# Performance work log

Measured on AMD Instinct MI355X. Metric: run time of the kernel, lower is better.

## Reference

```python
import jax, jax.numpy as jnp
import numpy as np

ND, ED, HD, L, K = 128, 64, 256, 4, 24   # node_dim, edge_dim(num_rbf), hidden_dim, num_layers, max_neighbors
CUTOFF = 8.0
N = 2048  # n_atoms


def _silu(x):
    return x * jax.nn.sigmoid(x)


def _lattice(lengths, angles):
    a, b, c = lengths[0], lengths[1], lengths[2]
    deg = jnp.asarray(np.pi / 180.0, lengths.dtype)
    al, be, ga = angles[0] * deg, angles[1] * deg, angles[2] * deg
    lx = a
    xy = b * jnp.cos(ga)
    xz = c * jnp.cos(be)
    ly = b * jnp.sin(ga)
    yz = (b * c * jnp.cos(al) - xy * xz) / ly
    lz = jnp.sqrt(c ** 2 - xz ** 2 - yz ** 2)
    z = jnp.zeros((), lengths.dtype)
    return jnp.stack([jnp.stack([lx, z, z]), jnp.stack([xy, ly, z]), jnp.stack([xz, yz, lz])])


def _rbf(d):
    centers = jnp.linspace(0.0, CUTOFF, ED)
    widths = jnp.full((ED,), CUTOFF / ED)
    d = d[..., None]
    g = jnp.exp(-(d - centers) ** 2 / (2.0 * widths ** 2))
    cv = 0.5 * (jnp.cos(d * jnp.pi / CUTOFF) + 1.0) * (d < CUTOFF).astype(d.dtype)
    return g * cv


def _forward(atom_types, frac_coords, lengths, angles, timesteps, emb, tW, tb,
             eW1, eb1, eW2, eb2, nW1, nb1, nW2, nb2, cW1, cb1, cW2, cb2):
    n = frac_coords.shape[0]
    lattice = _lattice(lengths, angles)            # [3,3]
    cart = frac_coords @ lattice                   # [n,3]

    # ---- vectorized periodic neighbor graph (replaces host triple loop) ----
    shifts = jnp.asarray(np.array([[i, j, k] for i in (-1, 0, 1) for j in (-1, 0, 1) for k in (-1, 0, 1)],
                                  dtype=np.float32))
    sv = shifts @ lattice                          # [27,3]
    p = cart[None, :, :] + sv[:, None, :]          # [27,n,3] shifted atom positions
    # squared distances without materializing [27,n,n,3]
    d2 = (p * p).sum(-1)[:, :, None] + (cart * cart).sum(-1)[None, None, :] \
         - 2.0 * jnp.einsum('snk,mk->snm', p, cart)      # [27, n_j, n_i]
    dist = jnp.sqrt(jnp.maximum(d2, 1e-12))
    cand = jnp.where((dist < CUTOFF) & (dist > 0.01), dist, jnp.inf)
    cand = cand.reshape(27 * n, n).T               # [n_i, 27*n_j]; flat f = s*n + j
    _, idx = jax.lax.top_k(-cand, K)               # K smallest distances per atom i
    d_k = jnp.take_along_axis(cand, idx, axis=1)   # [n,K]
    dst = (idx % n).reshape(-1)                    # neighbor atom j (edge_list = [i, j])
    src = jnp.repeat(jnp.arange(n), K)             # center atom i
    valid = jnp.isfinite(d_k).reshape(-1)
    m = valid.astype(jnp.float32)[:, None]         # [E,1] pad mask
    d_e = jnp.where(valid, d_k.reshape(-1), 0.0)
    edge_attr = _rbf(d_e)                          # [E, ED]

    # ---- EGNN stack ----
    nf = emb[atom_types] + timesteps @ tW + tb     # [n, ND]
    coords = cart
    seg = lambda x, i: jax.ops.segment_sum(x, i, num_segments=n)
    for l in range(L):
        ef = jnp.concatenate([nf[src], nf[dst], edge_attr], axis=-1)   # [E, 2*ND+ED]
        msg = _silu(_silu(ef @ eW1[l] + eb1[l]) @ eW2[l] + eb2[l])     # [E, HD]
        aggr = seg(msg * m, dst)                                       # [n, HD]
        nf = nf + _silu(jnp.concatenate([nf, aggr], axis=-1) @ nW1[l] + nb1[l]) @ nW2[l] + nb2[l]
        w = _silu(msg @ cW1[l] + cb1[l]) @ cW2[l] + cb2[l]             # [E,1]
        cd = coords[src] - coords[dst]
        cd = cd / (jnp.linalg.norm(cd, axis=-1, keepdims=True) + 1e-8)
        coords = coords + seg(w * cd * m, dst)
    return nf, coords


def setup_inputs() -> dict:
    key = jax.random.key(0)
    ks = jax.random.split(key, 16)
    pr = lambda k, shape: jax.random.normal(k, shape, jnp.float32) * 0.02
    return dict(
        atom_types=jax.random.randint(ks[0], (N,), 0, 100),
        frac_coords=jax.random.uniform(ks[1], (N, 3), jnp.float32),
        lengths=jnp.ones((3,), jnp.float32) * 12.0,
        angles=jnp.ones((3,), jnp.float32) * 90.0,
        timesteps=jax.random.normal(ks[2], (N, 128), jnp.float32),
        emb=pr(ks[3], (100, ND)),
        tW=pr(ks[4], (128, ND)), tb=jnp.zeros((ND,), jnp.float32),
        eW1=pr(ks[5], (L, 2 * ND + ED, HD)), eb1=jnp.zeros((L, HD), jnp.float32),
        eW2=pr(ks[6], (L, HD, HD)), eb2=jnp.zeros((L, HD), jnp.float32),
        nW1=pr(ks[7], (L, ND + HD, HD)), nb1=jnp.zeros((L, HD), jnp.float32),
        nW2=pr(ks[8], (L, HD, ND)), nb2=jnp.zeros((L, ND), jnp.float32),
        cW1=pr(ks[9], (L, HD, HD // 2)), cb1=jnp.zeros((L, HD // 2), jnp.float32),
        cW2=pr(ks[10], (L, HD // 2, 1)), cb2=jnp.zeros((L, 1), jnp.float32),
    )


def reference(atom_types, frac_coords, lengths, angles, timesteps, emb, tW, tb,
              eW1, eb1, eW2, eb2, nW1, nb1, nW2, nb2, cW1, cb1, cW2, cb2):
    return _forward(atom_types, frac_coords, lengths, angles, timesteps, emb, tW, tb,
                    eW1, eb1, eW2, eb2, nW1, nb1, nW2, nb2, cW1, cb1, cW2, cb2)
```

## Files before the change

### kernel.cpp

```cpp
#include <hip/hip_runtime.h>
#include <math.h>

#define NA 2048
#define KN 24
#define NE (NA*KN)
#define NDIM 128
#define EDIM 64
#define HDIM 256
#define NLAYER 4
#define MAXDEG 256
#define EB 64

typedef __attribute__((ext_vector_type(8))) short bf16x8;
typedef __attribute__((ext_vector_type(4))) float f32x4;

__device__ __forceinline__ float siluf(float x) {
    return __fdividef(x, 1.0f + __expf(-x));
}
__device__ __forceinline__ ushort f2b(float x) {
    unsigned u = __float_as_uint(x);
    return (ushort)((u + 0x7fffu + ((u >> 16) & 1u)) >> 16);
}
__device__ __forceinline__ float b2f(ushort h) { return __uint_as_float(((unsigned)h) << 16); }

__device__ __forceinline__ void gl_lds(const void* g, void* lds) {
    __builtin_amdgcn_global_load_lds(
        (const __attribute__((address_space(1))) unsigned int*)g,
        (__attribute__((address_space(3))) unsigned int*)lds, 16, 0, 0);
}

struct Lat { float lx, xy, xz, ly, yz, lz; };

__device__ __forceinline__ Lat make_lattice(const float* lengths, const float* angles) {
    const float deg = 0.017453292519943295f;
    float a = lengths[0], b = lengths[1], c = lengths[2];
    float al = angles[0]*deg, be = angles[1]*deg, ga = angles[2]*deg;
    Lat L;
    L.lx = a;
    L.xy = b * cosf(ga);
    L.xz = c * cosf(be);
    L.ly = b * sinf(ga);
    L.yz = (b*c*cosf(al) - L.xy*L.xz) / L.ly;
    L.lz = sqrtf(c*c - L.xz*L.xz - L.yz*L.yz);
    return L;
}

__global__ void setup_kernel(const float* __restrict__ frac, const float* __restrict__ lengths,
                             const float* __restrict__ angles, float* __restrict__ cart,
                             float* __restrict__ cxg, float* __restrict__ cyg,
                             float* __restrict__ czg, float* __restrict__ sv,
                             int* __restrict__ ccnt) {
    int i = blockIdx.x*blockDim.x + threadIdx.x;
    Lat L = make_lattice(lengths, angles);
    if (i < NA) {
        float f0 = frac[i*3], f1 = frac[i*3+1], f2 = frac[i*3+2];
        float x = f0*L.lx + f1*L.xy + f2*L.xz;
        float y = f1*L.ly + f2*L.yz;
        float z = f2*L.lz;
        cart[i*3+0] = x; cart[i*3+1] = y; cart[i*3+2] = z;
        cxg[i] = x; cyg[i] = y; czg[i] = z;
        ccnt[i] = 0;
    }
    if (i < 27) {
        float s0 = (float)(i/9 - 1), s1 = (float)((i/3)%3 - 1), s2 = (float)(i%3 - 1);
        sv[i*3+0] = s0*L.lx + s1*L.xy + s2*L.xz;
        sv[i*3+1] = s1*L.ly + s2*L.yz;
        sv[i*3+2] = s2*L.lz;
    }
}

__global__ __launch_bounds__(64) void knn_kernel(
        const float* __restrict__ cxg, const float* __restrict__ cyg,
        const float* __restrict__ czg, const float* __restrict__ lengths,
        const float* __restrict__ angles, const float* __restrict__ sv,
        int* __restrict__ dstl, ushort* __restrict__ rbf16,
        int* __restrict__ ccnt, int* __restrict__ cedg) {
    __shared__ float sd2L[16][64];
    __shared__ int   sfL[16][64];
    const int lane = threadIdx.x;
    const int i = blockIdx.x;
    Lat L = make_lattice(lengths, angles);
    const float deg = 0.017453292519943295f;
    const bool ortho = fabsf(cosf(angles[0]*deg)) < 1e-6f &&
                       fabsf(cosf(angles[1]*deg)) < 1e-6f &&
                       fabsf(cosf(angles[2]*deg)) < 1e-6f;
    const float cx = cxg[i], cy = cyg[i], cz = czg[i];
    const float invlx = 1.0f/L.lx, invly = 1.0f/L.ly, invlz = 1.0f/L.lz;
    float R = 2.8f;
    int mycnt = 0, cnt = 0;
    bool flatm = false;
    for (int attempt = 0; attempt < 8; ++attempt) {
        const float R2 = R*R;
        mycnt = 0;
        flatm = !ortho || (attempt == 7);
        if (!flatm) {
#pragma unroll 2
            for (int j0 = 0; j0 < NA; j0 += 64) {
                const int j = j0 + lane;
                const float dx = cxg[j] - cx, dy = cyg[j] - cy, dz = czg[j] - cz;
                const float kx = rintf(dx*invlx), ky = rintf(dy*invly), kz = rintf(dz*invlz);
                const float ex = dx - (kx*L.lx + ky*L.xy + kz*L.xz);
                const float ey = dy - (ky*L.ly + kz*L.yz);
                const float ez = dz - kz*L.lz;
                const float d2 = fmaf(ex,ex,fmaf(ey,ey,ez*ez));
                if (d2 < R2 && d2 > 1e-4f) {
                    const int s = (1-(int)kx)*9 + (1-(int)ky)*3 + (1-(int)kz);
                    if (mycnt < 16) { sd2L[mycnt][lane] = d2; sfL[mycnt][lane] = (s<<11) + j; }
                    ++mycnt;
                }
            }
            if (__ballot(mycnt > 16)) {
                flatm = true;
            } else {
                int tot = mycnt;
                for (int off = 32; off > 0; off >>= 1) tot += __shfl_xor(tot, off, 64);
                cnt = tot;
            }
        }
        if (flatm) {
            cnt = 0;
            for (int s = 0; s < 27; ++s) {
                const float svx = sv[s*3], svy = sv[s*3+1], svz = sv[s*3+2];
                for (int j0 = 0; j0 < NA; j0 += 64) {
                    const int j = j0 + lane;
                    const float ex = cxg[j] + svx - cx;
                    const float ey = cyg[j] + svy - cy;
                    const float ez = czg[j] + svz - cz;
                    const float d2 = fmaf(ex,ex,fmaf(ey,ey,ez*ez));
                    const bool hit = (d2 < R2) && (d2 > 1e-4f);
                    const unsigned long long m = __ballot(hit);
                    const int rank = __popcll(m & ((1ull<<lane)-1ull));
                    const int slot = cnt + rank;
                    if (hit && slot < 1024) { sd2L[slot>>6][slot&63] = d2; sfL[slot>>6][slot&63] = (s<<11)+j; }
                    cnt += __popcll(m);
                }
            }
            cnt = min(cnt, 1024);
        }
        if (cnt >= KN) break;
        R = fminf(R*1.6f, flatm ? 8.0f : 5.9f);
    }
    int vq;
    if (flatm) vq = (lane < cnt) ? min(16, ((cnt - 1 - lane) >> 6) + 1) : 0;
    else       vq = mycnt;
    unsigned long long key[16];
#pragma unroll
    for (int q = 0; q < 16; ++q) {
        const float d2v = sd2L[q][lane];
        const int fl = sfL[q][lane];
        const unsigned long long kk = ((unsigned long long)__float_as_uint(d2v) << 20)
                                    | ((unsigned long long)(unsigned)fl << 4) | (unsigned)q;
        key[q] = (q < vq) ? kk : ~0ull;
    }
    float der[KN];
    for (int k = 0; k < KN; ++k) {
        unsigned long long lm = key[0];
#pragma unroll
        for (int q = 1; q < 16; ++q) lm = key[q] < lm ? key[q] : lm;
        for (int off = 32; off > 0; off >>= 1) {
            unsigned long long o = __shfl_xor(lm, off, 64);
            lm = o < lm ? o : lm;
        }
        der[k] = sqrtf(__uint_as_float((unsigned)(lm >> 20)));
        if (lane == 0) {
            const int jn = (int)((lm >> 4) & 2047u);
            dstl[i*KN + k] = jn;
            const int slot = atomicAdd(&ccnt[jn], 1);
            if (slot < MAXDEG) cedg[(size_t)jn*MAXDEG + slot] = i*KN + k;
        }
#pragma unroll
        for (int q = 0; q < 16; ++q) if (key[q] == lm) key[q] = ~0ull;
    }
    const float center = (8.0f/63.0f) * (float)lane;
    for (int k = 0; k < KN; ++k) {
        const float d = der[k];
        const float diff = d - center;
        const float g = __expf(diff*diff * -32.0f);
        const float cv = 0.5f * (__cosf(d * (float)(M_PI/8.0)) + 1.0f);
        rbf16[(size_t)(i*KN + k)*EDIM + lane] = f2b(g * cv);
    }
}

__global__ void csort_kernel(const int* __restrict__ ccnt, int* __restrict__ cedg) {
    const int j = blockIdx.x*4 + (threadIdx.x >> 6);
    const int lane = threadIdx.x & 63;
    const int cnt = min(ccnt[j], MAXDEG);
    if (cnt <= 64) {
        int v = (lane < cnt) ? cedg[(size_t)j*MAXDEG + lane] : 0x7FFFFFFF;
#pragma unroll
        for (int k = 2; k <= 64; k <<= 1) {
#pragma unroll
            for (int s = k >> 1; s > 0; s >>= 1) {
                int o = __shfl_xor(v, s, 64);
                const bool up = ((lane & k) == 0);
                const bool lowhalf = ((lane & s) == 0);
                v = ((lowhalf == up) ? min(v, o) : max(v, o));
            }
        }
        if (lane < cnt) cedg[(size_t)j*MAXDEG + lane] = v;
    } else if (lane == 0) {
        int* L = cedg + (size_t)j*MAXDEG;
        for (int a = 1; a < cnt; ++a) {
            int v = L[a]; int b = a - 1;
            while (b >= 0 && L[b] > v) { L[b+1] = L[b]; --b; }
            L[b+1] = v;
        }
    }
}

__global__ void nf_init_kernel(const int* __restrict__ atom_types, const float* __restrict__ ts,
                               const float* __restrict__ emb, const float* __restrict__ tW,
                               const float* __restrict__ tb, float* __restrict__ nf,
                               ushort* __restrict__ nf16) {
    int i = blockIdx.x, c = threadIdx.x;
    float acc = emb[atom_types[i]*NDIM + c] + tb[c];
    for (int kk = 0; kk < 128; ++kk) acc += ts[i*128 + kk] * tW[kk*NDIM + c];
    nf[i*NDIM + c] = acc;
    nf16[i*NDIM + c] = f2b(acc);
}

__global__ void wprep_all(const float* __restrict__ eW1, const float* __restrict__ eW2,
                          const float* __restrict__ cW1, const float* __restrict__ nW1,
                          const float* __restrict__ nW2,
                          ushort* __restrict__ eW1t, ushort* __restrict__ eW2t,
                          ushort* __restrict__ cW1t, ushort* __restrict__ nW1t,
                          ushort* __restrict__ nW2t) {
    __shared__ float tile[64][65];
    const int b = blockIdx.x;
    const float* W; ushort* Wt; int Kk, Nn, rel;
    if (b < 80)       { W = eW1; Wt = eW1t; Kk = 320; Nn = 256; rel = b; }
    else if (b < 144) { W = eW2; Wt = eW2t; Kk = 256; Nn = 256; rel = b - 80; }
    else if (b < 176) { W = cW1; Wt = cW1t; Kk = 256; Nn = 128; rel = b - 144; }
    else if (b < 272) { W = nW1; Wt = nW1t; Kk = 384; Nn = 256; rel = b - 176; }
    else              { W = nW2; Wt = nW2t; Kk = 256; Nn = 128; rel = b - 272; }
    const int kt = Kk >> 6, nt = Nn >> 6, per = kt*nt;
    const int l = rel / per, r2 = rel - l*per;
    const int k0 = (r2 / nt) * 64, n0 = (r2 - (r2/nt)*nt) * 64;
    const float* Wl = W + (size_t)l*Kk*Nn;
    ushort* Wtl = Wt + (size_t)l*Kk*Nn;
    const int tr = threadIdx.x >> 6, tc = threadIdx.x & 63;
#pragma unroll
    for (int q = 0; q < 16; ++q) {
        const int k = q*4 + tr;
        tile[k][tc] = Wl[(size_t)(k0 + k)*Nn + n0 + tc];
    }
    __syncthreads();
#pragma unroll
    for (int q = 0; q < 16; ++q) {
        const int n = q*4 + tr;
        Wtl[(size_t)(n0 + n)*Kk + k0 + tc] = f2b(tile[tc][n]);
    }
}

__global__ __launch_bounds__(256) void edge_fused(
        const ushort* __restrict__ nf16, const int* __restrict__ dstl,
        const ushort* __restrict__ rbf16,
        const ushort* __restrict__ eW1t,
        const ushort* __restrict__ eW2t,
        const ushort* __restrict__ cW1t,
        const float* __restrict__ eb1, const float* __restrict__ eb2,
        const float* __restrict__ cb1, const float* __restrict__ cW2v,
        const float* __restrict__ cb2v,
        ushort* __restrict__ msg16, float* __restrict__ wvout) {
    __shared__ alignas(16) char R0[40960];
    __shared__ alignas(16) char R1[32768];
    __shared__ int sdst[64];
    __shared__ float wred[2][64];
    ushort* As = (ushort*)R0;
    ushort* Bs = (ushort*)(R0 + 8192);
    ushort* B2 = (ushort*)R1;
    ushort* Cs = (ushort*)R1;

    const int t = threadIdx.x, wave = t >> 6, lane = t & 63;
    const int row0 = blockIdx.x*EB;
    if (t < EB) sdst[t] = dstl[row0 + t];
    __syncthreads();
    const int wr = (wave >> 1)*32;
    const int wcB = (wave & 1)*128;
    const int lr = lane & 15, g0 = lane >> 4;

    const int rA_  = wave*16 + (lane >> 2);
    const int gA_  = (lane & 3) ^ ((rA_ >> 1) & 3);
    const int eA_  = row0 + rA_;
    const ushort* baseSrc = nf16  + (size_t)(eA_/KN)*NDIM + gA_*8;
    const ushort* baseDst = nf16  + (size_t)sdst[rA_]*NDIM + gA_*8;
    const ushort* baseRbf = rbf16 + (size_t)eA_*EDIM + gA_*8;
    const uint ldsA_ = (uint)(wave*16)*32;
    const ushort* baseW1[4]; const ushort* baseW2[4];
    uint ldsBq[4];
#pragma unroll
    for (int q = 0; q < 4; ++q) {
        const int rowb = wave*64 + q*16 + (lane >> 2);
        const int gB = (lane & 3) ^ ((rowb >> 1) & 3);
        baseW1[q] = eW1t + (size_t)rowb*320 + gB*8;
        baseW2[q] = eW2t + (size_t)rowb*256 + gB*8;
        ldsBq[q] = (uint)(wave*64 + q*16)*32;
    }
    const ushort* baseC[2];
    uint ldsCq[2];
#pragma unroll
    for (int q = 0; q < 2; ++q) {
        const int rowb = wave*32 + q*16 + (lane >> 2);
        const int gB = (lane & 3) ^ ((rowb >> 1) & 3);
        baseC[q] = cW1t + (size_t)rowb*256 + gB*8;
        ldsCq[q] = (uint)(wave*32 + q*16)*32;
    }

    auto STAGEA = [&](int buf, int k0) {
        const ushort* gp = (k0 < NDIM) ? baseSrc + k0
                         : (k0 < 2*NDIM) ? baseDst + (k0 - NDIM)
                         : baseRbf + (k0 - 2*NDIM);
        gl_lds(gp, As + (size_t)buf*2048 + ldsA_);
#pragma unroll
        for (int q = 0; q < 4; ++q)
            gl_lds(baseW1[q] + k0, Bs + (size_t)buf*8192 + ldsBq[q]);
    };
    f32x4 acc[2][8];
#pragma unroll
    for (int m = 0; m < 2; ++m)
#pragma unroll
        for (int n = 0; n < 8; ++n) acc[m][n] = (f32x4){0.f,0.f,0.f,0.f};
    STAGEA(0, 0);
    int cur = 0;
#pragma unroll
    for (int it = 0; it < 10; ++it) {
        if (it + 1 < 10) {
            STAGEA(cur ^ 1, (it + 1)*32);
            asm volatile("s_waitcnt vmcnt(5)" ::: "memory");
        } else {
            asm volatile("s_waitcnt vmcnt(0)" ::: "memory");
        }
        __builtin_amdgcn_s_barrier();
        bf16x8 af[2], bfr[8];
#pragma unroll
        for (int m = 0; m < 2; ++m) {
            const int rA = wr + m*16 + lr;
            af[m] = *reinterpret_cast<const bf16x8*>(&As[cur*2048 + rA*32 + ((g0 ^ ((rA>>1)&3)))*8]);
        }
#pragma unroll
        for (int n = 0; n < 8; ++n) {
            const int rB = wcB + n*16 + lr;
            bfr[n] = *reinterpret_cast<const bf16x8*>(&Bs[(size_t)cur*8192 + rB*32 + ((g0 ^ ((rB>>1)&3)))*8]);
        }
        __builtin_amdgcn_s_setprio(1);
#pragma unroll
        for (int m = 0; m < 2; ++m)
#pragma unroll
            for (int n = 0; n < 8; ++n)
                acc[m][n] = __builtin_amdgcn_mfma_f32_16x16x32_bf16(af[m], bfr[n], acc[m][n], 0, 0, 0);
        __builtin_amdgcn_s_setprio(0);
        asm volatile("s_waitcnt lgkmcnt(0)" ::: "memory");
        __builtin_amdgcn_s_barrier();
        cur ^= 1;
    }
    {
#pragma unroll
        for (int q = 0; q < 4; ++q)
            gl_lds(baseW2[q], B2 + ldsBq[q]);
    }
#pragma unroll
    for (int n = 0; n < 8; ++n) {
        const int cc = wcB + n*16 + lr;
        const float b1 = eb1[cc];
#pragma unroll
        for (int m = 0; m < 2; ++m) {
#pragma unroll
            for (int j = 0; j < 4; ++j) {
                const int rr = wr + m*16 + g0*4 + j;
                const float x = siluf(acc[m][n][j] + b1);
                *(ushort*)(R0 + rr*512 + ((cc*2) ^ ((rr&7)<<4))) = f2b(x);
            }
        }
    }
    __syncthreads();

#pragma unroll
    for (int m = 0; m < 2; ++m)
#pragma unroll
        for (int n = 0; n < 8; ++n) acc[m][n] = (f32x4){0.f,0.f,0.f,0.f};
    cur = 0;
#pragma unroll
    for (int it = 0; it < 8; ++it) {
        if (it + 1 < 8) {
            const int k0 = (it + 1)*32;
#pragma unroll
            for (int q = 0; q < 4; ++q)
                gl_lds(baseW2[q] + k0, B2 + (size_t)(cur^1)*8192 + ldsBq[q]);
            asm volatile("s_waitcnt vmcnt(4)" ::: "memory");
        } else {
            asm volatile("s_waitcnt vmcnt(0)" ::: "memory");
        }
        __builtin_amdgcn_s_barrier();
        bf16x8 af[2], bfr[8];
#pragma unroll
        for (int m = 0; m < 2; ++m) {
            const int rA = wr + m*16 + lr;
            const int kc = it*4 + g0;
            af[m] = *reinterpret_cast<const bf16x8*>(R0 + rA*512 + ((kc*16) ^ ((rA&7)<<4)));
        }
#pragma unroll
        for (int n = 0; n < 8; ++n) {
            const int rB = wcB + n*16 + lr;
            bfr[n] = *reinterpret_cast<const bf16x8*>(&B2[(size_t)cur*8192 + rB*32 + ((g0 ^ ((rB>>1)&3)))*8]);
        }
        __builtin_amdgcn_s_setprio(1);
#pragma unroll
        for (int m = 0; m < 2; ++m)
#pragma unroll
            for (int n = 0; n < 8; ++n)
                acc[m][n] = __builtin_amdgcn_mfma_f32_16x16x32_bf16(af[m], bfr[n], acc[m][n], 0, 0, 0);
        __builtin_amdgcn_s_setprio(0);
        asm volatile("s_waitcnt lgkmcnt(0)" ::: "memory");
        __builtin_amdgcn_s_barrier();
        cur ^= 1;
    }
    {
#pragma unroll
        for (int q = 0; q < 2; ++q)
            gl_lds(baseC[q], Cs + ldsCq[q]);
    }
#pragma unroll
    for (int n = 0; n < 8; ++n) {
        const int cc = wcB + n*16 + lr;
        const float b2 = eb2[cc];
#pragma unroll
        for (int m = 0; m < 2; ++m) {
#pragma unroll
            for (int j = 0; j < 4; ++j) {
                const int rr = wr + m*16 + g0*4 + j;
                *(ushort*)(R0 + rr*512 + ((cc*2) ^ ((rr&7)<<4))) = f2b(siluf(acc[m][n][j] + b2));
            }
        }
    }
    __syncthreads();

    const int wcC = (wave & 1)*64;
    f32x4 acc3[2][4];
#pragma unroll
    for (int m = 0; m < 2; ++m)
#pragma unroll
        for (int n = 0; n < 4; ++n) acc3[m][n] = (f32x4){0.f,0.f,0.f,0.f};
    cur = 0;
#pragma unroll
    for (int it = 0; it < 8; ++it) {
        if (it + 1 < 8) {
            const int k0 = (it + 1)*32;
#pragma unroll
            for (int q = 0; q < 2; ++q)
                gl_lds(baseC[q] + k0, Cs + (size_t)(cur^1)*4096 + ldsCq[q]);
            asm volatile("s_waitcnt vmcnt(2)" ::: "memory");
        } else {
            asm volatile("s_waitcnt vmcnt(0)" ::: "memory");
        }
        __builtin_amdgcn_s_barrier();
        bf16x8 af[2], bfr[4];
#pragma unroll
        for (int m = 0; m < 2; ++m) {
            const int rA = wr + m*16 + lr;
            const int kc = it*4 + g0;
            af[m] = *reinterpret_cast<const bf16x8*>(R0 + rA*512 + ((kc*16) ^ ((rA&7)<<4)));
        }
#pragma unroll
        for (int n = 0; n < 4; ++n) {
            const int rB = wcC + n*16 + lr;
            bfr[n] = *reinterpret_cast<const bf16x8*>(&Cs[(size_t)cur*4096 + rB*32 + ((g0 ^ ((rB>>1)&3)))*8]);
        }
        __builtin_amdgcn_s_setprio(1);
#pragma unroll
        for (int m = 0; m < 2; ++m)
#pragma unroll
            for (int n = 0; n < 4; ++n)
                acc3[m][n] = __builtin_amdgcn_mfma_f32_16x16x32_bf16(af[m], bfr[n], acc3[m][n], 0, 0, 0);
        __builtin_amdgcn_s_setprio(0);
        asm volatile("s_waitcnt lgkmcnt(0)" ::: "memory");
        __builtin_amdgcn_s_barrier();
        cur ^= 1;
    }
    float part[2][4];
#pragma unroll
    for (int m = 0; m < 2; ++m)
#pragma unroll
        for (int j = 0; j < 4; ++j) part[m][j] = 0.0f;
#pragma unroll
    for (int n = 0; n < 4; ++n) {
        const int cc = wcC + n*16 + lr;
        const float bb = cb1[cc];
        const float cw = cW2v[cc];
#pragma unroll
        for (int m = 0; m < 2; ++m)
#pragma unroll
            for (int j = 0; j < 4; ++j)
                part[m][j] += siluf(acc3[m][n][j] + bb) * cw;
    }
#pragma unroll
    for (int off = 1; off < 16; off <<= 1)
#pragma unroll
        for (int m = 0; m < 2; ++m)
#pragma unroll
            for (int j = 0; j < 4; ++j)
                part[m][j] += __shfl_xor(part[m][j], off, 64);
    if (lr == 0) {
#pragma unroll
        for (int m = 0; m < 2; ++m)
#pragma unroll
            for (int j = 0; j < 4; ++j)
                wred[wave & 1][wr + m*16 + g0*4 + j] = part[m][j];
    }
    __syncthreads();
    if (t < EB) wvout[row0 + t] = wred[0][t] + wred[1][t] + cb2v[0];
#pragma unroll
    for (int k = 0; k < 8; ++k) {
        const int off = (t + k*256) * 16;
        const int row = off >> 9;
        const int cg = ((off >> 4) & 31) ^ (row & 7);
        uint4 v = *reinterpret_cast<const uint4*>(R0 + off);
        *reinterpret_cast<uint4*>(msg16 + (size_t)(row0 + row)*256 + cg*8) = v;
    }
}

__global__ __launch_bounds__(256) void nodefused(
        const ushort* __restrict__ nf16, const ushort* __restrict__ aggr16,
        const ushort* __restrict__ nW1t,
        const ushort* __restrict__ nW2t,
        const float* __restrict__ nb1, const float* __restrict__ nb2,
        float* __restrict__ nf, ushort* __restrict__ nf16out) {
    __shared__ alignas(16) ushort Ab[12*2048];
    __shared__ alignas(16) char HsB[32768];
    __shared__ alignas(16) ushort Bs[2][256*32];
    const int t = threadIdx.x, wave = t >> 6, lane = t & 63;
    const int r0 = blockIdx.x*64;
    const int wr = (wave >> 1)*32;
    const int wcB = (wave & 1)*128;
    const int lr = lane & 15, g0 = lane >> 4;

#pragma unroll
    for (int c = 0; c < 3; ++c) {
        const int ks = wave*3 + c;
#pragma unroll
        for (int q = 0; q < 4; ++q) {
            const int r = q*16 + (lane >> 2);
            const int g = (lane & 3) ^ ((r >> 1) & 3);
            const int col = ks*32 + g*8;
            const ushort* gp = (col < NDIM)
                ? nf16 + (size_t)(r0 + r)*NDIM + col
                : aggr16 + (size_t)(r0 + r)*HDIM + (col - NDIM);
            gl_lds(gp, Ab + ks*2048 + q*16*32);
        }
    }
    const ushort* baseW1[4];
    uint ldsBq[4];
#pragma unroll
    for (int q = 0; q < 4; ++q) {
        const int rowb = wave*64 + q*16 + (lane >> 2);
        const int gB = (lane & 3) ^ ((rowb >> 1) & 3);
        baseW1[q] = nW1t + (size_t)rowb*384 + gB*8;
        ldsBq[q] = (uint)(wave*64 + q*16)*32;
    }
    const ushort* baseW2[2];
    uint ldsCq[2];
#pragma unroll
    for (int q = 0; q < 2; ++q) {
        const int rowb = wave*32 + q*16 + (lane >> 2);
        const int gB = (lane & 3) ^ ((rowb >> 1) & 3);
        baseW2[q] = nW2t + (size_t)rowb*256 + gB*8;
        ldsCq[q] = (uint)(wave*32 + q*16)*32;
    }
#pragma unroll
    for (int q = 0; q < 4; ++q)
        gl_lds(baseW1[q], &Bs[0][ldsBq[q]]);
    asm volatile("s_waitcnt vmcnt(0)" ::: "memory");
    __builtin_amdgcn_s_barrier();

    f32x4 acc[2][8];
#pragma unroll
    for (int m = 0; m < 2; ++m)
#pragma unroll
        for (int n = 0; n < 8; ++n) acc[m][n] = (f32x4){0.f,0.f,0.f,0.f};
    int cur = 0;
#pragma unroll
    for (int it = 0; it < 12; ++it) {
        if (it + 1 < 12) {
            const int k0 = (it + 1)*32;
#pragma unroll
            for (int q = 0; q < 4; ++q)
                gl_lds(baseW1[q] + k0, &Bs[cur^1][ldsBq[q]]);
            asm volatile("s_waitcnt vmcnt(4)" ::: "memory");
        } else {
            asm volatile("s_waitcnt vmcnt(0)" ::: "memory");
        }
        __builtin_amdgcn_s_barrier();
        bf16x8 af[2], bfr[8];
#pragma unroll
        for (int m = 0; m < 2; ++m) {
            const int rA = wr + m*16 + lr;
            af[m] = *reinterpret_cast<const bf16x8*>(&Ab[it*2048 + rA*32 + ((g0 ^ ((rA>>1)&3)))*8]);
        }
#pragma unroll
        for (int n = 0; n < 8; ++n) {
            const int rB = wcB + n*16 + lr;
            bfr[n] = *reinterpret_cast<const bf16x8*>(&Bs[cur][rB*32 + ((g0 ^ ((rB>>1)&3)))*8]);
        }
        __builtin_amdgcn_s_setprio(1);
#pragma unroll
        for (int m = 0; m < 2; ++m)
#pragma unroll
            for (int n = 0; n < 8; ++n)
                acc[m][n] = __builtin_amdgcn_mfma_f32_16x16x32_bf16(af[m], bfr[n], acc[m][n], 0, 0, 0);
        __builtin_amdgcn_s_setprio(0);
        asm volatile("s_waitcnt lgkmcnt(0)" ::: "memory");
        __builtin_amdgcn_s_barrier();
        cur ^= 1;
    }
#pragma unroll
    for (int q = 0; q < 2; ++q)
        gl_lds(baseW2[q], &Bs[0][ldsCq[q]]);
#pragma unroll
    for (int n = 0; n < 8; ++n) {
        const int cc = wcB + n*16 + lr;
        const float b1 = nb1[cc];
#pragma unroll
        for (int m = 0; m < 2; ++m) {
#pragma unroll
            for (int j = 0; j < 4; ++j) {
                const int rr = wr + m*16 + g0*4 + j;
                *(ushort*)(HsB + rr*512 + ((cc*2) ^ ((rr&7)<<4))) = f2b(siluf(acc[m][n][j] + b1));
            }
        }
    }
    __syncthreads();

    const int wcC = (wave & 1)*64;
    f32x4 acc3[2][4];
#pragma unroll
    for (int m = 0; m < 2; ++m)
#pragma unroll
        for (int n = 0; n < 4; ++n) acc3[m][n] = (f32x4){0.f,0.f,0.f,0.f};
    cur = 0;
#pragma unroll
    for (int it = 0; it < 8; ++it) {
        if (it + 1 < 8) {
            const int k0 = (it + 1)*32;
#pragma unroll
            for (int q = 0; q < 2; ++q)
                gl_lds(baseW2[q] + k0, &Bs[cur^1][ldsCq[q]]);
            asm volatile("s_waitcnt vmcnt(2)" ::: "memory");
        } else {
            asm volatile("s_waitcnt vmcnt(0)" ::: "memory");
        }
        __builtin_amdgcn_s_barrier();
        bf16x8 af[2], bfr[4];
#pragma unroll
        for (int m = 0; m < 2; ++m) {
            const int rA = wr + m*16 + lr;
            const int kc = it*4 + g0;
            af[m] = *reinterpret_cast<const bf16x8*>(HsB + rA*512 + ((kc*16) ^ ((rA&7)<<4)));
        }
#pragma unroll
        for (int n = 0; n < 4; ++n) {
            const int rB = wcC + n*16 + lr;
            bfr[n] = *reinterpret_cast<const bf16x8*>(&Bs[cur][rB*32 + ((g0 ^ ((rB>>1)&3)))*8]);
        }
        __builtin_amdgcn_s_setprio(1);
#pragma unroll
        for (int m = 0; m < 2; ++m)
#pragma unroll
            for (int n = 0; n < 4; ++n)
                acc3[m][n] = __builtin_amdgcn_mfma_f32_16x16x32_bf16(af[m], bfr[n], acc3[m][n], 0, 0, 0);
        __builtin_amdgcn_s_setprio(0);
        asm volatile("s_waitcnt lgkmcnt(0)" ::: "memory");
        __builtin_amdgcn_s_barrier();
        cur ^= 1;
    }
#pragma unroll
    for (int n = 0; n < 4; ++n) {
        const int cc = wcC + n*16 + lr;
        const float b2 = nb2[cc];
#pragma unroll
        for (int m = 0; m < 2; ++m) {
#pragma unroll
            for (int j = 0; j < 4; ++j) {
                const int rr = r0 + wr + m*16 + g0*4 + j;
                float x = acc3[m][n][j] + b2 + nf[(size_t)rr*NDIM + cc];
                nf[(size_t)rr*NDIM + cc] = x;
                nf16out[(size_t)rr*NDIM + cc] = f2b(x);
            }
        }
    }
}

__global__ void node_kernel(const ushort* __restrict__ msg16, const float* __restrict__ cold,
                            const float* __restrict__ wv, const int* __restrict__ ccnt,
                            const int* __restrict__ cedg,
                            ushort* __restrict__ aggr16, float* __restrict__ cnew) {
    __shared__ int se[4][64];
    const int w = threadIdx.x >> 6, lane = threadIdx.x & 63;
    const int j = blockIdx.x*4 + w;
    const int cnt = min(ccnt[j], MAXDEG);
    se[w][lane] = (lane < cnt) ? cedg[(size_t)j*MAXDEG + lane] : 0;
    __syncthreads();
    const int c4 = lane*4;
    float s0 = 0, s1 = 0, s2 = 0, s3 = 0;
    const int lim = min(cnt, 64);
    for (int q = 0; q < lim; ++q) {
        const int e = se[w][q];
        ushort4 v = *reinterpret_cast<const ushort4*>(&msg16[(size_t)e*HDIM + c4]);
        s0 += b2f(v.x); s1 += b2f(v.y); s2 += b2f(v.z); s3 += b2f(v.w);
    }
    for (int q = 64; q < cnt; ++q) {
        const int e = cedg[(size_t)j*MAXDEG + q];
        ushort4 v = *reinterpret_cast<const ushort4*>(&msg16[(size_t)e*HDIM + c4]);
        s0 += b2f(v.x); s1 += b2f(v.y); s2 += b2f(v.z); s3 += b2f(v.w);
    }
    ushort4 o; o.x = f2b(s0); o.y = f2b(s1); o.z = f2b(s2); o.w = f2b(s3);
    *reinterpret_cast<ushort4*>(&aggr16[(size_t)j*HDIM + c4]) = o;
    const float jx = cold[j*3], jy = cold[j*3+1], jz = cold[j*3+2];
    float dx = 0, dy = 0, dz = 0;
    for (int q = lane; q < cnt; q += 64) {
        const int e = (q < 64) ? se[w][q] : cedg[(size_t)j*MAXDEG + q];
        const int si = e / KN;
        const float ax = cold[si*3]   - jx;
        const float ay = cold[si*3+1] - jy;
        const float az = cold[si*3+2] - jz;
        const float inv = wv[e] / (sqrtf(ax*ax + ay*ay + az*az) + 1e-8f);
        dx += inv*ax; dy += inv*ay; dz += inv*az;
    }
    for (int off = 32; off > 0; off >>= 1) {
        dx += __shfl_xor(dx, off, 64);
        dy += __shfl_xor(dy, off, 64);
        dz += __shfl_xor(dz, off, 64);
    }
    if (lane == 0) {
        cnew[j*3]   = jx + dx;
        cnew[j*3+1] = jy + dy;
        cnew[j*3+2] = jz + dz;
    }
}

__global__ void copyout_kernel(const float* __restrict__ nf, const float* __restrict__ coords,
                               float* __restrict__ out) {
    int idx = blockIdx.x*256 + threadIdx.x;
    if (idx < NA*NDIM) out[idx] = nf[idx];
    else if (idx < NA*NDIM + NA*3) out[idx] = coords[idx - NA*NDIM];
}

extern "C" void kernel_launch(void* const* d_in, const int* in_sizes, int n_in,
                              void* d_out, int out_size, void* d_ws, size_t ws_size,
                              hipStream_t stream) {
    const int*   atom_types = (const int*)  d_in[0];
    const float* frac       = (const float*)d_in[1];
    const float* lengths    = (const float*)d_in[2];
    const float* angles     = (const float*)d_in[3];
    const float* timesteps  = (const float*)d_in[4];
    const float* emb        = (const float*)d_in[5];
    const float* tW         = (const float*)d_in[6];
    const float* tb         = (const float*)d_in[7];
    const float* eW1        = (const float*)d_in[8];
    const float* eb1        = (const float*)d_in[9];
    const float* eW2        = (const float*)d_in[10];
    const float* eb2        = (const float*)d_in[11];
    const float* nW1        = (const float*)d_in[12];
    const float* nb1        = (const float*)d_in[13];
    const float* nW2        = (const float*)d_in[14];
    const float* nb2        = (const float*)d_in[15];
    const float* cW1        = (const float*)d_in[16];
    const float* cb1        = (const float*)d_in[17];
    const float* cW2        = (const float*)d_in[18];
    const float* cb2        = (const float*)d_in[19];

    char* p = (char*)d_ws;
    auto alloc = [&](size_t bytes) { char* q = p; p += (bytes + 255) & ~(size_t)255; return q; };
    float*  sv    = (float*) alloc(81*4);
    float*  c0    = (float*) alloc((size_t)NA*3*4);
    float*  c1    = (float*) alloc((size_t)NA*3*4);
    float*  cxg   = (float*) alloc((size_t)NA*4);
    float*  cyg   = (float*) alloc((size_t)NA*4);
    float*  czg   = (float*) alloc((size_t)NA*4);
    float*  nf    = (float*) alloc((size_t)NA*NDIM*4);
    int*    dstl  = (int*)   alloc((size_t)NE*4);
    ushort* rbf16 = (ushort*)alloc((size_t)NE*EDIM*2);
    int*    ccnt  = (int*)   alloc((size_t)NA*4);
    int*    cedg  = (int*)   alloc((size_t)NA*MAXDEG*4);
    ushort* aggr16= (ushort*)alloc((size_t)NA*HDIM*2);
    float*  wv    = (float*) alloc((size_t)NE*4);
    ushort* nf16  = (ushort*)alloc((size_t)NA*NDIM*2);
    ushort* msg16 = (ushort*)alloc((size_t)NE*HDIM*2);
    ushort* eW1t  = (ushort*)alloc((size_t)NLAYER*(2*NDIM+EDIM)*HDIM*2);
    ushort* eW2t  = (ushort*)alloc((size_t)NLAYER*HDIM*HDIM*2);
    ushort* cW1t  = (ushort*)alloc((size_t)NLAYER*(HDIM/2)*HDIM*2);
    ushort* nW1t  = (ushort*)alloc((size_t)NLAYER*(NDIM+HDIM)*HDIM*2);
    ushort* nW2t  = (ushort*)alloc((size_t)NLAYER*HDIM*NDIM*2);

    setup_kernel<<<8, 256, 0, stream>>>(frac, lengths, angles, c0, cxg, cyg, czg, sv, ccnt);
    knn_kernel<<<NA, 64, 0, stream>>>(cxg, cyg, czg, lengths, angles, sv,
                                      dstl, rbf16, ccnt, cedg);
    csort_kernel<<<NA/4, 256, 0, stream>>>(ccnt, cedg);
    nf_init_kernel<<<NA, 128, 0, stream>>>(atom_types, timesteps, emb, tW, tb, nf, nf16);
    wprep_all<<<304, 256, 0, stream>>>(eW1, eW2, cW1, nW1, nW2,
                                       eW1t, eW2t, cW1t, nW1t, nW2t);

    float* cin = c0; float* cout = c1;
    for (int l = 0; l < NLAYER; ++l) {
        const float* eb1l = eb1 + (size_t)l*HDIM;
        const float* eb2l = eb2 + (size_t)l*HDIM;
        const float* nb1l = nb1 + (size_t)l*HDIM;
        const float* nb2l = nb2 + (size_t)l*NDIM;
        const float* cb1l = cb1 + (size_t)l*(HDIM/2);
        const float* cW2l = cW2 + (size_t)l*(HDIM/2);
        const float* cb2l = cb2 + (size_t)l;

        edge_fused<<<NE/EB, 256, 0, stream>>>(
            nf16, dstl, rbf16,
            eW1t + (size_t)l*(2*NDIM+EDIM)*HDIM, eW2t + (size_t)l*HDIM*HDIM,
            cW1t + (size_t)l*(HDIM/2)*HDIM,
            eb1l, eb2l, cb1l, cW2l, cb2l, msg16, wv);
        node_kernel<<<NA/4, 256, 0, stream>>>(msg16, cin, wv, ccnt, cedg, aggr16, cout);
        nodefused<<<NA/64, 256, 0, stream>>>(
            nf16, aggr16, nW1t + (size_t)l*(NDIM+HDIM)*HDIM, nW2t + (size_t)l*HDIM*NDIM,
            nb1l, nb2l, nf, nf16);
        float* tmp = cin; cin = cout; cout = tmp;
    }
    copyout_kernel<<<(NA*NDIM + NA*3)/256, 256, 0, stream>>>(nf, cin, (float*)d_out);
}
```

Before: 368.2 us.

## Single-buffer edge_fused LDS staging to cut shared memory per block

Replaces the double-buffered global-to-LDS prefetch in all three GEMM stages of edge_fused with single buffers. Each loop now waits for all loads, computes, and only then issues the next tile's load. This shrinks LDS from about 73KB to about 49KB per block so more blocks can be resident per CU. In exchange, load latency is no longer overlapped with MFMA work inside a block and must be hidden by the extra resident blocks instead.

```diff
diff --git a/kernel.cpp b/kernel.cpp
--- a/kernel.cpp
+++ b/kernel.cpp
@@ -262,8 +262,8 @@
         const float* __restrict__ cb1, const float* __restrict__ cW2v,
         const float* __restrict__ cb2v,
         ushort* __restrict__ msg16, float* __restrict__ wvout) {
-    __shared__ alignas(16) char R0[40960];
-    __shared__ alignas(16) char R1[32768];
+    __shared__ alignas(16) char R0[32768];
+    __shared__ alignas(16) char R1[16384];
     __shared__ int sdst[64];
     __shared__ float wred[2][64];
     ushort* As = (ushort*)R0;
@@ -306,41 +306,35 @@
         ldsCq[q] = (uint)(wave*32 + q*16)*32;
     }
 
-    auto STAGEA = [&](int buf, int k0) {
+    auto STAGEA = [&](int k0) {
         const ushort* gp = (k0 < NDIM) ? baseSrc + k0
                          : (k0 < 2*NDIM) ? baseDst + (k0 - NDIM)
                          : baseRbf + (k0 - 2*NDIM);
-        gl_lds(gp, As + (size_t)buf*2048 + ldsA_);
+        gl_lds(gp, As + ldsA_);
 #pragma unroll
         for (int q = 0; q < 4; ++q)
-            gl_lds(baseW1[q] + k0, Bs + (size_t)buf*8192 + ldsBq[q]);
+            gl_lds(baseW1[q] + k0, Bs + ldsBq[q]);
     };
     f32x4 acc[2][8];
 #pragma unroll
     for (int m = 0; m < 2; ++m)
 #pragma unroll
         for (int n = 0; n < 8; ++n) acc[m][n] = (f32x4){0.f,0.f,0.f,0.f};
-    STAGEA(0, 0);
-    int cur = 0;
+    STAGEA(0);
 #pragma unroll
     for (int it = 0; it < 10; ++it) {
-        if (it + 1 < 10) {
-            STAGEA(cur ^ 1, (it + 1)*32);
-            asm volatile("s_waitcnt vmcnt(5)" ::: "memory");
-        } else {
-            asm volatile("s_waitcnt vmcnt(0)" ::: "memory");
-        }
+        asm volatile("s_waitcnt vmcnt(0)" ::: "memory");
         __builtin_amdgcn_s_barrier();
         bf16x8 af[2], bfr[8];
 #pragma unroll
         for (int m = 0; m < 2; ++m) {
             const int rA = wr + m*16 + lr;
-            af[m] = *reinterpret_cast<const bf16x8*>(&As[cur*2048 + rA*32 + ((g0 ^ ((rA>>1)&3)))*8]);
+            af[m] = *reinterpret_cast<const bf16x8*>(&As[rA*32 + ((g0 ^ ((rA>>1)&3)))*8]);
         }
 #pragma unroll
         for (int n = 0; n < 8; ++n) {
             const int rB = wcB + n*16 + lr;
-            bfr[n] = *reinterpret_cast<const bf16x8*>(&Bs[(size_t)cur*8192 + rB*32 + ((g0 ^ ((rB>>1)&3)))*8]);
+            bfr[n] = *reinterpret_cast<const bf16x8*>(&Bs[rB*32 + ((g0 ^ ((rB>>1)&3)))*8]);
         }
         __builtin_amdgcn_s_setprio(1);
 #pragma unroll
@@ -351,7 +345,7 @@
         __builtin_amdgcn_s_setprio(0);
         asm volatile("s_waitcnt lgkmcnt(0)" ::: "memory");
         __builtin_amdgcn_s_barrier();
-        cur ^= 1;
+        if (it + 1 < 10) STAGEA((it + 1)*32);
     }
     {
 #pragma unroll
@@ -378,18 +372,9 @@
     for (int m = 0; m < 2; ++m)
 #pragma unroll
         for (int n = 0; n < 8; ++n) acc[m][n] = (f32x4){0.f,0.f,0.f,0.f};
-    cur = 0;
 #pragma unroll
     for (int it = 0; it < 8; ++it) {
-        if (it + 1 < 8) {
-            const int k0 = (it + 1)*32;
-#pragma unroll
-            for (int q = 0; q < 4; ++q)
-                gl_lds(baseW2[q] + k0, B2 + (size_t)(cur^1)*8192 + ldsBq[q]);
-            asm volatile("s_waitcnt vmcnt(4)" ::: "memory");
-        } else {
-            asm volatile("s_waitcnt vmcnt(0)" ::: "memory");
-        }
+        asm volatile("s_waitcnt vmcnt(0)" ::: "memory");
         __builtin_amdgcn_s_barrier();
         bf16x8 af[2], bfr[8];
 #pragma unroll
@@ -401,7 +386,7 @@
 #pragma unroll
         for (int n = 0; n < 8; ++n) {
             const int rB = wcB + n*16 + lr;
-            bfr[n] = *reinterpret_cast<const bf16x8*>(&B2[(size_t)cur*8192 + rB*32 + ((g0 ^ ((rB>>1)&3)))*8]);
+            bfr[n] = *reinterpret_cast<const bf16x8*>(&B2[rB*32 + ((g0 ^ ((rB>>1)&3)))*8]);
         }
         __builtin_amdgcn_s_setprio(1);
 #pragma unroll
@@ -412,7 +397,12 @@
         __builtin_amdgcn_s_setprio(0);
         asm volatile("s_waitcnt lgkmcnt(0)" ::: "memory");
         __builtin_amdgcn_s_barrier();
-        cur ^= 1;
+        if (it + 1 < 8) {
+            const int k0 = (it + 1)*32;
+#pragma unroll
+            for (int q = 0; q < 4; ++q)
+                gl_lds(baseW2[q] + k0, B2 + ldsBq[q]);
+        }
     }
     {
 #pragma unroll
@@ -440,18 +430,9 @@
     for (int m = 0; m < 2; ++m)
 #pragma unroll
         for (int n = 0; n < 4; ++n) acc3[m][n] = (f32x4){0.f,0.f,0.f,0.f};
-    cur = 0;
 #pragma unroll
     for (int it = 0; it < 8; ++it) {
-        if (it + 1 < 8) {
-            const int k0 = (it + 1)*32;
-#pragma unroll
-            for (int q = 0; q < 2; ++q)
-                gl_lds(baseC[q] + k0, Cs + (size_t)(cur^1)*4096 + ldsCq[q]);
-            asm volatile("s_waitcnt vmcnt(2)" ::: "memory");
-        } else {
-            asm volatile("s_waitcnt vmcnt(0)" ::: "memory");
-        }
+        asm volatile("s_waitcnt vmcnt(0)" ::: "memory");
         __builtin_amdgcn_s_barrier();
         bf16x8 af[2], bfr[4];
 #pragma unroll
@@ -463,7 +444,7 @@
 #pragma unroll
         for (int n = 0; n < 4; ++n) {
             const int rB = wcC + n*16 + lr;
-            bfr[n] = *reinterpret_cast<const bf16x8*>(&Cs[(size_t)cur*4096 + rB*32 + ((g0 ^ ((rB>>1)&3)))*8]);
+            bfr[n] = *reinterpret_cast<const bf16x8*>(&Cs[rB*32 + ((g0 ^ ((rB>>1)&3)))*8]);
         }
         __builtin_amdgcn_s_setprio(1);
 #pragma unroll
@@ -474,7 +455,12 @@
         __builtin_amdgcn_s_setprio(0);
         asm volatile("s_waitcnt lgkmcnt(0)" ::: "memory");
         __builtin_amdgcn_s_barrier();
-        cur ^= 1;
+        if (it + 1 < 8) {
+            const int k0 = (it + 1)*32;
+#pragma unroll
+            for (int q = 0; q < 2; ++q)
+                gl_lds(baseC[q] + k0, Cs + ldsCq[q]);
+        }
     }
     float part[2][4];
 #pragma unroll
```

Result: slower. 378.5 us (+2.8%).
